# Kernel tuning notes

Measured on AMD Instinct MI355X. Metric: run time of the kernel, lower is better.

Reference implementation:

```python
import jax, jax.numpy as jnp
import numpy as np

N_P = 128          # n_particles
N_D = 3            # spatial dims (dim // n_particles)
DIM = N_P * N_D    # 384
F = 32             # n_features
H = 32             # n_hidden
B = 128            # batch
COORDS_RANGE = 5.0
EPS = 1e-6         # bgflow distances_from_vectors eps


def _edge_indices():
    # i-major ordering over all ordered pairs (i, j), i != j, matching
    # both _create_edges_indices and the off-diagonal layout of distance_vectors.
    ii, jj = np.meshgrid(np.arange(N_P), np.arange(N_P), indexing='ij')
    mask = ii != jj
    return ii[mask], jj[mask]  # each [E] with E = N_P*(N_P-1)

IDX_I, IDX_J = _edge_indices()


def setup_inputs() -> dict:
    key = jax.random.key(0)
    ks = jax.random.split(key, 12)

    def nrm(k, shape, s=0.05):
        return jax.random.normal(k, shape, jnp.float32) * s

    return dict(
        x=jax.random.normal(ks[0], (B, DIM), jnp.float32),
        h=jax.random.normal(ks[1], (B, N_P, F), jnp.float32),
        d_static=jax.random.uniform(ks[2], (B, N_P * (N_P - 1)), jnp.float32),
        # edge_network: Linear(2F+2, H), SiLU, Linear(H, F), SiLU
        e_w1=nrm(ks[3], (2 * F + 2, H)), e_b1=jnp.zeros((H,), jnp.float32),
        e_w2=nrm(ks[4], (H, F)), e_b2=jnp.zeros((F,), jnp.float32),
        # node_network: Linear(2F, H), SiLU, Linear(H, F)
        n_w1=nrm(ks[5], (2 * F, H)), n_b1=jnp.zeros((H,), jnp.float32),
        n_w2=nrm(ks[6], (H, F)), n_b2=jnp.zeros((F,), jnp.float32),
        # coord_network: Linear(F, H), SiLU, Linear(H, 1, bias=False) [xavier gain 1e-3], Tanh
        c_w1=nrm(ks[7], (F, H)), c_b1=jnp.zeros((H,), jnp.float32),
        c_w2=nrm(ks[8], (H, 1), 0.001),
        # att_mlp: Linear(F, 1), Sigmoid
        a_w=nrm(ks[9], (F, 1)), a_b=jnp.zeros((1,), jnp.float32),
    )


def reference(x, h, d_static, e_w1, e_b1, e_w2, e_b2,
              n_w1, n_b1, n_w2, n_b2, c_w1, c_b1, c_w2, a_w, a_b):
    xi = x.reshape(-1, N_P, N_D)                       # [B, n, 3]
    # distance_vectors: r_ij = x_i - x_j over ordered pairs, diagonal removed
    r = xi[:, IDX_I] - xi[:, IDX_J]                    # [B, E, 3]
    d = jnp.sqrt(jnp.sum(r * r, axis=-1) + EPS)        # [B, E]

    # edge_transformation on [h_i, h_j, d^2, d_static^2]
    hi = h[:, IDX_I]                                   # [B, E, F] gather
    hj = h[:, IDX_J]                                   # [B, E, F] gather
    ds = d_static.reshape(d.shape)
    e_in = jnp.concatenate([hi, hj, (d * d)[..., None], (ds * ds)[..., None]], axis=-1)
    m = jax.nn.silu(jax.nn.silu(e_in @ e_w1 + e_b1) @ e_w2 + e_b2)  # [B, E, F]
    m = m * jax.nn.sigmoid(m @ a_w + a_b)              # attention gate

    # coordinate update: r / (d + 1) * tanh(coord_mlp(m)), summed over neighbors
    trans = jnp.tanh(jax.nn.silu(m @ c_w1 + c_b1) @ c_w2)           # [B, E, 1]
    x_upd = (r / (d[..., None] + 1.0)) * trans                      # [B, E, 3]
    x_upd = x_upd.reshape(-1, N_P, N_P - 1, N_D).sum(axis=2)        # scatter-sum over j
    x_out = xi + x_upd * COORDS_RANGE                               # [B, n, 3]

    # node update: sum messages over neighbors, concat with h, small MLP
    m_i = m.reshape(-1, N_P, N_P - 1, F).sum(axis=2)                # [B, n, F]
    h_upd = jax.nn.silu(jnp.concatenate([h, m_i], axis=-1) @ n_w1 + n_b1) @ n_w2 + n_b2
    h_out = h + h_upd
    return x_out, h_out
```

## Files before the change

kernel.cpp:

```cpp
#include <hip/hip_runtime.h>
#include <hip/hip_bf16.h>

#define NP 128
#define NPE 127

typedef short v8s __attribute__((ext_vector_type(8)));
typedef float v4f __attribute__((ext_vector_type(4)));

#define L_HCJ  0
#define L_GEOM 4608
#define L_HCI  8704
#define L_TOT  8832

__device__ __forceinline__ float fast_rcp(float x){ return __builtin_amdgcn_rcpf(x); }
__device__ __forceinline__ float sigmoidf_(float x){ return fast_rcp(1.0f + __expf(-x)); }
__device__ __forceinline__ float siluf(float x){ return x * sigmoidf_(x); }
__device__ __forceinline__ float tanhf_fast(float x){
    return 1.0f - 2.0f * fast_rcp(1.0f + __expf(2.0f * x));
}
__device__ __forceinline__ short f2bf(float x){
    __hip_bfloat16 h = __float2bfloat16(x);
    return *reinterpret_cast<short*>(&h);
}

__global__ __launch_bounds__(256)
void eq_gnn_fused(const float* __restrict__ X, const float* __restrict__ Hin,
                  const float* __restrict__ DS,
                  const float* __restrict__ EW1, const float* __restrict__ EB1,
                  const float* __restrict__ EW2, const float* __restrict__ EB2,
                  const float* __restrict__ NW1, const float* __restrict__ NB1,
                  const float* __restrict__ NW2, const float* __restrict__ NB2,
                  const float* __restrict__ CW1, const float* __restrict__ CB1,
                  const float* __restrict__ CW2,
                  const float* __restrict__ AW,  const float* __restrict__ AB,
                  float* __restrict__ OUT)
{
    __shared__ float sm[L_TOT];
    const int tid  = threadIdx.x;
    const int lane = tid & 63;
    const int wid  = tid >> 6;
    const int m16  = lane & 15;
    const int q    = lane >> 4;
    const int bI   = blockIdx.x >> 5;
    const int grp  = blockIdx.x & 31;
    const int i    = grp * 4 + wid;
    const int node = bI * 128 + i;

    {
        v8s Aj0, Aj1;
        #pragma unroll
        for (int jj = 0; jj < 8; ++jj){
            Aj0[jj] = f2bf(EW1[(32 + q*8 + jj) * 32 + m16]);
            Aj1[jj] = f2bf(EW1[(32 + q*8 + jj) * 32 + 16 + m16]);
        }
        #pragma unroll
        for (int rr = 0; rr < 2; ++rr){
            const int row = (wid * 2 + rr) * 16 + m16;
            const float* hp = &Hin[(bI * 128 + row) * 32 + q * 8];
            const float4 h0 = *(const float4*)&hp[0];
            const float4 h1 = *(const float4*)&hp[4];
            v8s Bh;
            Bh[0]=f2bf(h0.x); Bh[1]=f2bf(h0.y); Bh[2]=f2bf(h0.z); Bh[3]=f2bf(h0.w);
            Bh[4]=f2bf(h1.x); Bh[5]=f2bf(h1.y); Bh[6]=f2bf(h1.z); Bh[7]=f2bf(h1.w);
            v4f d0 = {0.f,0.f,0.f,0.f}, d1 = {0.f,0.f,0.f,0.f};
            d0 = __builtin_amdgcn_mfma_f32_16x16x32_bf16(Aj0, Bh, d0, 0, 0, 0);
            d1 = __builtin_amdgcn_mfma_f32_16x16x32_bf16(Aj1, Bh, d1, 0, 0, 0);
            #pragma unroll
            for (int r = 0; r < 4; ++r){
                sm[L_HCJ + row * 36 + q*4 + r]      = d0[r];
                sm[L_HCJ + row * 36 + 16 + q*4 + r] = d1[r];
            }
        }
    }
    if (tid < 128){
        const int nl = tid >> 5, o = tid & 31;
        const float* hp = &Hin[(bI * 128 + grp * 4 + nl) * 32];
        float acc = EB1[o];
        #pragma unroll
        for (int k = 0; k < 32; ++k) acc = fmaf(hp[k], EW1[k * 32 + o], acc);
        sm[L_HCI + nl * 32 + o] = acc;
    }
    float* sg = &sm[L_GEOM + wid * 1024];
    const float xi0 = X[bI*384 + i*3 + 0];
    const float xi1 = X[bI*384 + i*3 + 1];
    const float xi2 = X[bI*384 + i*3 + 2];
    #pragma unroll
    for (int p = 0; p < 2; ++p){
        const int slot = lane + 64 * p;
        const int js = (slot < NPE) ? slot : 126;
        const int j = js + ((js >= i) ? 1 : 0);
        const float* xj = &X[bI*384 + j*3];
        const float r0 = xi0 - xj[0], r1 = xi1 - xj[1], r2 = xi2 - xj[2];
        const float d2 = fmaf(r0, r0, fmaf(r1, r1, fmaf(r2, r2, 1e-6f)));
        const float d  = sqrtf(d2);
        const float rinv = fast_rcp(d + 1.0f);
        const float dsv = DS[bI*16256 + i*127 + js];
        *(float4*)&sg[slot*8]     = make_float4(r0, r1, r2, rinv);
        *(float2*)&sg[slot*8 + 4] = make_float2(d2, dsv * dsv);
    }
    __syncthreads();

    v8s Aw20, Aw21, Ac0, Ac1;
    #pragma unroll
    for (int jj = 0; jj < 8; ++jj){
        Aw20[jj] = f2bf(EW2[(q*8 + jj) * 32 + m16]);
        Aw21[jj] = f2bf(EW2[(q*8 + jj) * 32 + 16 + m16]);
        const int tau = (jj < 4) ? (q*4 + jj) : (16 + q*4 + (jj - 4));
        Ac0[jj] = f2bf(CW1[tau * 32 + m16]);
        Ac1[jj] = f2bf(CW1[tau * 32 + 16 + m16]);
    }
    const float4 w64a = *(const float4*)&EW1[64*32 + q*8];
    const float4 w64b = *(const float4*)&EW1[64*32 + q*8 + 4];
    const float4 w65a = *(const float4*)&EW1[65*32 + q*8];
    const float4 w65b = *(const float4*)&EW1[65*32 + q*8 + 4];
    const float4 b2A = *(const float4*)&EB2[q*4];
    const float4 b2B = *(const float4*)&EB2[16 + q*4];
    const float4 cbA = *(const float4*)&CB1[q*4];
    const float4 cbB = *(const float4*)&CB1[16 + q*4];
    const float4 cwA = *(const float4*)&CW2[q*4];
    const float4 cwB = *(const float4*)&CW2[16 + q*4];
    const float4 awA = *(const float4*)&AW[q*4];
    const float4 awB = *(const float4*)&AW[16 + q*4];
    const float ab0 = AB[0];
    const float4 hci0 = *(const float4*)&sm[L_HCI + wid*32 + q*8];
    const float4 hci1 = *(const float4*)&sm[L_HCI + wid*32 + q*8 + 4];

    float ms[8];
    #pragma unroll
    for (int jj = 0; jj < 8; ++jj) ms[jj] = 0.f;
    float xc0 = 0.f, xc1 = 0.f, xc2 = 0.f;

    #pragma unroll 1
    for (int tl = 0; tl < 8; ++tl){
        const int e = tl * 16 + m16;
        const float valid = (e < NPE) ? 1.f : 0.f;
        const int js = (e < NPE) ? e : 126;
        const int j = js + ((js >= i) ? 1 : 0);

        const float2 dd = *(const float2*)&sg[e*8 + 4];
        const float4 hj0 = *(const float4*)&sm[L_HCJ + j*36 + q*8];
        const float4 hj1 = *(const float4*)&sm[L_HCJ + j*36 + q*8 + 4];

        v8s Bt;
        Bt[0] = f2bf(siluf(fmaf(dd.x, w64a.x, fmaf(dd.y, w65a.x, hci0.x + hj0.x))));
        Bt[1] = f2bf(siluf(fmaf(dd.x, w64a.y, fmaf(dd.y, w65a.y, hci0.y + hj0.y))));
        Bt[2] = f2bf(siluf(fmaf(dd.x, w64a.z, fmaf(dd.y, w65a.z, hci0.z + hj0.z))));
        Bt[3] = f2bf(siluf(fmaf(dd.x, w64a.w, fmaf(dd.y, w65a.w, hci0.w + hj0.w))));
        Bt[4] = f2bf(siluf(fmaf(dd.x, w64b.x, fmaf(dd.y, w65b.x, hci1.x + hj1.x))));
        Bt[5] = f2bf(siluf(fmaf(dd.x, w64b.y, fmaf(dd.y, w65b.y, hci1.y + hj1.y))));
        Bt[6] = f2bf(siluf(fmaf(dd.x, w64b.z, fmaf(dd.y, w65b.z, hci1.z + hj1.z))));
        Bt[7] = f2bf(siluf(fmaf(dd.x, w64b.w, fmaf(dd.y, w65b.w, hci1.w + hj1.w))));

        v4f c0 = {b2A.x, b2A.y, b2A.z, b2A.w};
        v4f c1 = {b2B.x, b2B.y, b2B.z, b2B.w};
        c0 = __builtin_amdgcn_mfma_f32_16x16x32_bf16(Aw20, Bt, c0, 0, 0, 0);
        c1 = __builtin_amdgcn_mfma_f32_16x16x32_bf16(Aw21, Bt, c1, 0, 0, 0);
        const float s0 = siluf(c0[0]), s1 = siluf(c0[1]), s2 = siluf(c0[2]), s3 = siluf(c0[3]);
        const float s4 = siluf(c1[0]), s5 = siluf(c1[1]), s6 = siluf(c1[2]), s7 = siluf(c1[3]);

        float lg = s0*awA.x + s1*awA.y + s2*awA.z + s3*awA.w
                 + s4*awB.x + s5*awB.y + s6*awB.z + s7*awB.w;
        lg += __shfl_xor(lg, 16, 64);
        lg += __shfl_xor(lg, 32, 64);
        const float att = sigmoidf_(lg + ab0) * valid;

        v8s Bm;
        float g;
        g = s0*att; ms[0] += g; Bm[0] = f2bf(g);
        g = s1*att; ms[1] += g; Bm[1] = f2bf(g);
        g = s2*att; ms[2] += g; Bm[2] = f2bf(g);
        g = s3*att; ms[3] += g; Bm[3] = f2bf(g);
        g = s4*att; ms[4] += g; Bm[4] = f2bf(g);
        g = s5*att; ms[5] += g; Bm[5] = f2bf(g);
        g = s6*att; ms[6] += g; Bm[6] = f2bf(g);
        g = s7*att; ms[7] += g; Bm[7] = f2bf(g);

        v4f e0 = {cbA.x, cbA.y, cbA.z, cbA.w};
        v4f e1 = {cbB.x, cbB.y, cbB.z, cbB.w};
        e0 = __builtin_amdgcn_mfma_f32_16x16x32_bf16(Ac0, Bm, e0, 0, 0, 0);
        e1 = __builtin_amdgcn_mfma_f32_16x16x32_bf16(Ac1, Bm, e1, 0, 0, 0);
        float tr = siluf(e0[0])*cwA.x + siluf(e0[1])*cwA.y + siluf(e0[2])*cwA.z + siluf(e0[3])*cwA.w
                 + siluf(e1[0])*cwB.x + siluf(e1[1])*cwB.y + siluf(e1[2])*cwB.z + siluf(e1[3])*cwB.w;
        tr += __shfl_xor(tr, 16, 64);
        tr += __shfl_xor(tr, 32, 64);

        const float4 rv = *(const float4*)&sg[e*8];
        const float coef = tanhf_fast(tr) * rv.w * valid;
        xc0 = fmaf(rv.x, coef, xc0);
        xc1 = fmaf(rv.y, coef, xc1);
        xc2 = fmaf(rv.z, coef, xc2);
    }

    #pragma unroll
    for (int jj = 0; jj < 8; ++jj){
        float v = ms[jj];
        v += __shfl_xor(v, 1, 64); v += __shfl_xor(v, 2, 64);
        v += __shfl_xor(v, 4, 64); v += __shfl_xor(v, 8, 64);
        ms[jj] = v;
    }
    {
        float v0 = xc0, v1 = xc1, v2 = xc2;
        #pragma unroll
        for (int s = 1; s < 64; s <<= 1){
            v0 += __shfl_xor(v0, s, 64);
            v1 += __shfl_xor(v1, s, 64);
            v2 += __shfl_xor(v2, s, 64);
        }
        xc0 = v0 * 0.25f; xc1 = v1 * 0.25f; xc2 = v2 * 0.25f;
    }

    if (lane < 3){
        const float xiv = (lane == 0) ? xi0 : ((lane == 1) ? xi1 : xi2);
        const float xcv = (lane == 0) ? xc0 : ((lane == 1) ? xc1 : xc2);
        OUT[bI*384 + i*3 + lane] = fmaf(xcv, 5.0f, xiv);
    }

    if (m16 == 0){
        #pragma unroll
        for (int jj = 0; jj < 8; ++jj){
            const int tau = (jj < 4) ? (q*4 + jj) : (16 + q*4 + (jj - 4));
            sg[tau] = ms[jj];
        }
    }

    const int o = lane & 31;
    const float* hp = &Hin[node * 32];
    float a1 = NB1[o];
    #pragma unroll
    for (int k = 0; k < 32; ++k) a1 = fmaf(hp[k], NW1[k * 32 + o], a1);
    #pragma unroll
    for (int k = 0; k < 32; ++k) a1 = fmaf(sg[k], NW1[(32 + k) * 32 + o], a1);
    const float s1v = siluf(a1);
    float a2 = NB2[o];
    #pragma unroll
    for (int k = 0; k < 32; ++k) a2 = fmaf(__shfl(s1v, k, 64), NW2[k * 32 + o], a2);
    if (lane < 32)
        OUT[49152 + node * 32 + o] = hp[o] + a2;
}

extern "C" void kernel_launch(void* const* d_in, const int* in_sizes, int n_in,
                              void* d_out, int out_size, void* d_ws, size_t ws_size,
                              hipStream_t stream) {
    (void)in_sizes; (void)n_in; (void)out_size; (void)d_ws; (void)ws_size;
    eq_gnn_fused<<<dim3(4096), dim3(256), 0, stream>>>(
        (const float*)d_in[0],  (const float*)d_in[1],  (const float*)d_in[2],
        (const float*)d_in[3],  (const float*)d_in[4],  (const float*)d_in[5],  (const float*)d_in[6],
        (const float*)d_in[7],  (const float*)d_in[8],  (const float*)d_in[9],  (const float*)d_in[10],
        (const float*)d_in[11], (const float*)d_in[12], (const float*)d_in[13],
        (const float*)d_in[14], (const float*)d_in[15],
        (float*)d_out);
}
```

Before: 171.0 us.

## Use 8-wave blocks, packed float2 math, exp2-based activations, split geometry LDS

Blocks now hold 8 waves (8 nodes) instead of 4, so each block computes the per-batch h_j projection table once for twice as many nodes. This halves the redundant MFMA and global-load work for that table. The SiLU, attention and coord-MLP arithmetic is regrouped into float2 vectors so the compiler can emit packed FP32 instructions. Sigmoid and tanh now use a raw exp2 builtin, and geometry storage in LDS is split into separate r/rinv and d² arrays. The larger blocks use more shared memory and registers per block, which may reduce occupancy.

New measurement: 158.7 us. -7.2%, faster.

```diff
diff --git a/kernel.cpp b/kernel.cpp
--- a/kernel.cpp
+++ b/kernel.cpp
@@ -1,29 +1,48 @@
 #include <hip/hip_runtime.h>
 #include <hip/hip_bf16.h>
 
-#define NP 128
 #define NPE 127
 
 typedef short v8s __attribute__((ext_vector_type(8)));
 typedef float v4f __attribute__((ext_vector_type(4)));
-
-#define L_HCJ  0
-#define L_GEOM 4608
-#define L_HCI  8704
-#define L_TOT  8832
+typedef float v2f __attribute__((ext_vector_type(2)));
+
+#define L_HCJ 0
+#define L_HCI 4608
+#define L_GR  4864
+#define L_GD  8960
+#define L_TOT 11008
 
 __device__ __forceinline__ float fast_rcp(float x){ return __builtin_amdgcn_rcpf(x); }
-__device__ __forceinline__ float sigmoidf_(float x){ return fast_rcp(1.0f + __expf(-x)); }
-__device__ __forceinline__ float siluf(float x){ return x * sigmoidf_(x); }
+__device__ __forceinline__ float exp2_fast(float x){
+#if __has_builtin(__builtin_amdgcn_exp2f)
+    return __builtin_amdgcn_exp2f(x);
+#else
+    return exp2f(x);
+#endif
+}
+#define LOG2E 1.44269504f
+__device__ __forceinline__ float sigmoidf_(float x){
+    return fast_rcp(1.0f + exp2_fast(-LOG2E * x));
+}
 __device__ __forceinline__ float tanhf_fast(float x){
-    return 1.0f - 2.0f * fast_rcp(1.0f + __expf(2.0f * x));
+    return fmaf(-2.0f, fast_rcp(1.0f + exp2_fast(2.0f * LOG2E * x)), 1.0f);
+}
+__device__ __forceinline__ v2f splat2(float v){ v2f r; r.x = v; r.y = v; return r; }
+__device__ __forceinline__ v2f silu2(v2f x){
+    v2f t = x * splat2(-LOG2E);
+    v2f e; e.x = exp2_fast(t.x); e.y = exp2_fast(t.y);
+    v2f d = e + splat2(1.0f);
+    v2f r; r.x = fast_rcp(d.x); r.y = fast_rcp(d.y);
+    return x * r;
 }
 __device__ __forceinline__ short f2bf(float x){
     __hip_bfloat16 h = __float2bfloat16(x);
     return *reinterpret_cast<short*>(&h);
 }
-
-__global__ __launch_bounds__(256)
+union f4u { float4 f4; v2f v2[2]; float f[4]; };
+
+__global__ __launch_bounds__(512)
 void eq_gnn_fused(const float* __restrict__ X, const float* __restrict__ Hin,
                   const float* __restrict__ DS,
                   const float* __restrict__ EW1, const float* __restrict__ EB1,
@@ -41,9 +60,9 @@
     const int wid  = tid >> 6;
     const int m16  = lane & 15;
     const int q    = lane >> 4;
-    const int bI   = blockIdx.x >> 5;
-    const int grp  = blockIdx.x & 31;
-    const int i    = grp * 4 + wid;
+    const int bI   = blockIdx.x >> 4;
+    const int grp  = blockIdx.x & 15;
+    const int i    = grp * 8 + wid;
     const int node = bI * 128 + i;
 
     {
@@ -53,34 +72,32 @@
             Aj0[jj] = f2bf(EW1[(32 + q*8 + jj) * 32 + m16]);
             Aj1[jj] = f2bf(EW1[(32 + q*8 + jj) * 32 + 16 + m16]);
         }
-        #pragma unroll
-        for (int rr = 0; rr < 2; ++rr){
-            const int row = (wid * 2 + rr) * 16 + m16;
-            const float* hp = &Hin[(bI * 128 + row) * 32 + q * 8];
-            const float4 h0 = *(const float4*)&hp[0];
-            const float4 h1 = *(const float4*)&hp[4];
-            v8s Bh;
-            Bh[0]=f2bf(h0.x); Bh[1]=f2bf(h0.y); Bh[2]=f2bf(h0.z); Bh[3]=f2bf(h0.w);
-            Bh[4]=f2bf(h1.x); Bh[5]=f2bf(h1.y); Bh[6]=f2bf(h1.z); Bh[7]=f2bf(h1.w);
-            v4f d0 = {0.f,0.f,0.f,0.f}, d1 = {0.f,0.f,0.f,0.f};
-            d0 = __builtin_amdgcn_mfma_f32_16x16x32_bf16(Aj0, Bh, d0, 0, 0, 0);
-            d1 = __builtin_amdgcn_mfma_f32_16x16x32_bf16(Aj1, Bh, d1, 0, 0, 0);
-            #pragma unroll
-            for (int r = 0; r < 4; ++r){
-                sm[L_HCJ + row * 36 + q*4 + r]      = d0[r];
-                sm[L_HCJ + row * 36 + 16 + q*4 + r] = d1[r];
-            }
-        }
-    }
-    if (tid < 128){
+        const int row = wid * 16 + m16;
+        const float* hp = &Hin[(bI * 128 + row) * 32 + q * 8];
+        const float4 h0 = *(const float4*)&hp[0];
+        const float4 h1 = *(const float4*)&hp[4];
+        v8s Bh;
+        Bh[0]=f2bf(h0.x); Bh[1]=f2bf(h0.y); Bh[2]=f2bf(h0.z); Bh[3]=f2bf(h0.w);
+        Bh[4]=f2bf(h1.x); Bh[5]=f2bf(h1.y); Bh[6]=f2bf(h1.z); Bh[7]=f2bf(h1.w);
+        v4f d0 = {0.f,0.f,0.f,0.f}, d1 = {0.f,0.f,0.f,0.f};
+        d0 = __builtin_amdgcn_mfma_f32_16x16x32_bf16(Aj0, Bh, d0, 0, 0, 0);
+        d1 = __builtin_amdgcn_mfma_f32_16x16x32_bf16(Aj1, Bh, d1, 0, 0, 0);
+        #pragma unroll
+        for (int r = 0; r < 4; ++r){
+            sm[L_HCJ + row * 36 + q*4 + r]      = d0[r];
+            sm[L_HCJ + row * 36 + 16 + q*4 + r] = d1[r];
+        }
+    }
+    if (tid < 256){
         const int nl = tid >> 5, o = tid & 31;
-        const float* hp = &Hin[(bI * 128 + grp * 4 + nl) * 32];
+        const float* hp = &Hin[(bI * 128 + grp * 8 + nl) * 32];
         float acc = EB1[o];
         #pragma unroll
         for (int k = 0; k < 32; ++k) acc = fmaf(hp[k], EW1[k * 32 + o], acc);
         sm[L_HCI + nl * 32 + o] = acc;
     }
-    float* sg = &sm[L_GEOM + wid * 1024];
+    float* sgr = &sm[L_GR + wid * 512];
+    float* sgd = &sm[L_GD + wid * 256];
     const float xi0 = X[bI*384 + i*3 + 0];
     const float xi1 = X[bI*384 + i*3 + 1];
     const float xi2 = X[bI*384 + i*3 + 2];
@@ -95,8 +112,8 @@
         const float d  = sqrtf(d2);
         const float rinv = fast_rcp(d + 1.0f);
         const float dsv = DS[bI*16256 + i*127 + js];
-        *(float4*)&sg[slot*8]     = make_float4(r0, r1, r2, rinv);
-        *(float2*)&sg[slot*8 + 4] = make_float2(d2, dsv * dsv);
+        *(float4*)&sgr[slot*4] = make_float4(r0, r1, r2, rinv);
+        *(float2*)&sgd[slot*2] = make_float2(d2, dsv * dsv);
     }
     __syncthreads();
 
@@ -109,25 +126,26 @@
         Ac0[jj] = f2bf(CW1[tau * 32 + m16]);
         Ac1[jj] = f2bf(CW1[tau * 32 + 16 + m16]);
     }
-    const float4 w64a = *(const float4*)&EW1[64*32 + q*8];
-    const float4 w64b = *(const float4*)&EW1[64*32 + q*8 + 4];
-    const float4 w65a = *(const float4*)&EW1[65*32 + q*8];
-    const float4 w65b = *(const float4*)&EW1[65*32 + q*8 + 4];
+    f4u w64a, w64b, w65a, w65b, hcia, hcib, awa, awb, cwa, cwb;
+    w64a.f4 = *(const float4*)&EW1[64*32 + q*8];
+    w64b.f4 = *(const float4*)&EW1[64*32 + q*8 + 4];
+    w65a.f4 = *(const float4*)&EW1[65*32 + q*8];
+    w65b.f4 = *(const float4*)&EW1[65*32 + q*8 + 4];
+    hcia.f4 = *(const float4*)&sm[L_HCI + wid*32 + q*8];
+    hcib.f4 = *(const float4*)&sm[L_HCI + wid*32 + q*8 + 4];
+    awa.f4  = *(const float4*)&AW[q*4];
+    awb.f4  = *(const float4*)&AW[16 + q*4];
+    cwa.f4  = *(const float4*)&CW2[q*4];
+    cwb.f4  = *(const float4*)&CW2[16 + q*4];
     const float4 b2A = *(const float4*)&EB2[q*4];
     const float4 b2B = *(const float4*)&EB2[16 + q*4];
     const float4 cbA = *(const float4*)&CB1[q*4];
     const float4 cbB = *(const float4*)&CB1[16 + q*4];
-    const float4 cwA = *(const float4*)&CW2[q*4];
-    const float4 cwB = *(const float4*)&CW2[16 + q*4];
-    const float4 awA = *(const float4*)&AW[q*4];
-    const float4 awB = *(const float4*)&AW[16 + q*4];
     const float ab0 = AB[0];
-    const float4 hci0 = *(const float4*)&sm[L_HCI + wid*32 + q*8];
-    const float4 hci1 = *(const float4*)&sm[L_HCI + wid*32 + q*8 + 4];
-
-    float ms[8];
-    #pragma unroll
-    for (int jj = 0; jj < 8; ++jj) ms[jj] = 0.f;
+
+    v2f ms2[4];
+    #pragma unroll
+    for (int g = 0; g < 4; ++g) ms2[g] = splat2(0.f);
     float xc0 = 0.f, xc1 = 0.f, xc2 = 0.f;
 
     #pragma unroll 1
@@ -137,66 +155,95 @@
         const int js = (e < NPE) ? e : 126;
         const int j = js + ((js >= i) ? 1 : 0);
 
-        const float2 dd = *(const float2*)&sg[e*8 + 4];
-        const float4 hj0 = *(const float4*)&sm[L_HCJ + j*36 + q*8];
-        const float4 hj1 = *(const float4*)&sm[L_HCJ + j*36 + q*8 + 4];
-
+        const float2 dd = *(const float2*)&sgd[e*2];
+        f4u hjA, hjB;
+        hjA.f4 = *(const float4*)&sm[L_HCJ + j*36 + q*8];
+        hjB.f4 = *(const float4*)&sm[L_HCJ + j*36 + q*8 + 4];
+        const v2f d2s  = splat2(dd.x);
+        const v2f ds2s = splat2(dd.y);
+
+        v2f t01, t23, t45, t67;
+        {
+            v2f z;
+            z = hcia.v2[0] + hjA.v2[0];
+            z = __builtin_elementwise_fma(d2s, w64a.v2[0], z);
+            z = __builtin_elementwise_fma(ds2s, w65a.v2[0], z);
+            t01 = silu2(z);
+            z = hcia.v2[1] + hjA.v2[1];
+            z = __builtin_elementwise_fma(d2s, w64a.v2[1], z);
+            z = __builtin_elementwise_fma(ds2s, w65a.v2[1], z);
+            t23 = silu2(z);
+            z = hcib.v2[0] + hjB.v2[0];
+            z = __builtin_elementwise_fma(d2s, w64b.v2[0], z);
+            z = __builtin_elementwise_fma(ds2s, w65b.v2[0], z);
+            t45 = silu2(z);
+            z = hcib.v2[1] + hjB.v2[1];
+            z = __builtin_elementwise_fma(d2s, w64b.v2[1], z);
+            z = __builtin_elementwise_fma(ds2s, w65b.v2[1], z);
+            t67 = silu2(z);
+        }
         v8s Bt;
-        Bt[0] = f2bf(siluf(fmaf(dd.x, w64a.x, fmaf(dd.y, w65a.x, hci0.x + hj0.x))));
-        Bt[1] = f2bf(siluf(fmaf(dd.x, w64a.y, fmaf(dd.y, w65a.y, hci0.y + hj0.y))));
-        Bt[2] = f2bf(siluf(fmaf(dd.x, w64a.z, fmaf(dd.y, w65a.z, hci0.z + hj0.z))));
-        Bt[3] = f2bf(siluf(fmaf(dd.x, w64a.w, fmaf(dd.y, w65a.w, hci0.w + hj0.w))));
-        Bt[4] = f2bf(siluf(fmaf(dd.x, w64b.x, fmaf(dd.y, w65b.x, hci1.x + hj1.x))));
-        Bt[5] = f2bf(siluf(fmaf(dd.x, w64b.y, fmaf(dd.y, w65b.y, hci1.y + hj1.y))));
-        Bt[6] = f2bf(siluf(fmaf(dd.x, w64b.z, fmaf(dd.y, w65b.z, hci1.z + hj1.z))));
-        Bt[7] = f2bf(siluf(fmaf(dd.x, w64b.w, fmaf(dd.y, w65b.w, hci1.w + hj1.w))));
+        Bt[0]=f2bf(t01.x); Bt[1]=f2bf(t01.y); Bt[2]=f2bf(t23.x); Bt[3]=f2bf(t23.y);
+        Bt[4]=f2bf(t45.x); Bt[5]=f2bf(t45.y); Bt[6]=f2bf(t67.x); Bt[7]=f2bf(t67.y);
 
         v4f c0 = {b2A.x, b2A.y, b2A.z, b2A.w};
         v4f c1 = {b2B.x, b2B.y, b2B.z, b2B.w};
         c0 = __builtin_amdgcn_mfma_f32_16x16x32_bf16(Aw20, Bt, c0, 0, 0, 0);
         c1 = __builtin_amdgcn_mfma_f32_16x16x32_bf16(Aw21, Bt, c1, 0, 0, 0);
-        const float s0 = siluf(c0[0]), s1 = siluf(c0[1]), s2 = siluf(c0[2]), s3 = siluf(c0[3]);
-        const float s4 = siluf(c1[0]), s5 = siluf(c1[1]), s6 = siluf(c1[2]), s7 = siluf(c1[3]);
-
-        float lg = s0*awA.x + s1*awA.y + s2*awA.z + s3*awA.w
-                 + s4*awB.x + s5*awB.y + s6*awB.z + s7*awB.w;
+        v2f sa, sb, sc, sd;
+        { v2f z; z.x=c0[0]; z.y=c0[1]; sa = silu2(z); }
+        { v2f z; z.x=c0[2]; z.y=c0[3]; sb = silu2(z); }
+        { v2f z; z.x=c1[0]; z.y=c1[1]; sc = silu2(z); }
+        { v2f z; z.x=c1[2]; z.y=c1[3]; sd = silu2(z); }
+
+        v2f lgv = sa * awa.v2[0];
+        lgv = __builtin_elementwise_fma(sb, awa.v2[1], lgv);
+        lgv = __builtin_elementwise_fma(sc, awb.v2[0], lgv);
+        lgv = __builtin_elementwise_fma(sd, awb.v2[1], lgv);
+        float lg = lgv.x + lgv.y;
         lg += __shfl_xor(lg, 16, 64);
         lg += __shfl_xor(lg, 32, 64);
         const float att = sigmoidf_(lg + ab0) * valid;
-
+        const v2f atts = splat2(att);
+
+        const v2f g0 = sa * atts, g1 = sb * atts, g2 = sc * atts, g3 = sd * atts;
+        ms2[0] += g0; ms2[1] += g1; ms2[2] += g2; ms2[3] += g3;
         v8s Bm;
-        float g;
-        g = s0*att; ms[0] += g; Bm[0] = f2bf(g);
-        g = s1*att; ms[1] += g; Bm[1] = f2bf(g);
-        g = s2*att; ms[2] += g; Bm[2] = f2bf(g);
-        g = s3*att; ms[3] += g; Bm[3] = f2bf(g);
-        g = s4*att; ms[4] += g; Bm[4] = f2bf(g);
-        g = s5*att; ms[5] += g; Bm[5] = f2bf(g);
-        g = s6*att; ms[6] += g; Bm[6] = f2bf(g);
-        g = s7*att; ms[7] += g; Bm[7] = f2bf(g);
+        Bm[0]=f2bf(g0.x); Bm[1]=f2bf(g0.y); Bm[2]=f2bf(g1.x); Bm[3]=f2bf(g1.y);
+        Bm[4]=f2bf(g2.x); Bm[5]=f2bf(g2.y); Bm[6]=f2bf(g3.x); Bm[7]=f2bf(g3.y);
 
         v4f e0 = {cbA.x, cbA.y, cbA.z, cbA.w};
         v4f e1 = {cbB.x, cbB.y, cbB.z, cbB.w};
         e0 = __builtin_amdgcn_mfma_f32_16x16x32_bf16(Ac0, Bm, e0, 0, 0, 0);
         e1 = __builtin_amdgcn_mfma_f32_16x16x32_bf16(Ac1, Bm, e1, 0, 0, 0);
-        float tr = siluf(e0[0])*cwA.x + siluf(e0[1])*cwA.y + siluf(e0[2])*cwA.z + siluf(e0[3])*cwA.w
-                 + siluf(e1[0])*cwB.x + siluf(e1[1])*cwB.y + siluf(e1[2])*cwB.z + siluf(e1[3])*cwB.w;
+        v2f ca, cb, cc, cd;
+        { v2f z; z.x=e0[0]; z.y=e0[1]; ca = silu2(z); }
+        { v2f z; z.x=e0[2]; z.y=e0[3]; cb = silu2(z); }
+        { v2f z; z.x=e1[0]; z.y=e1[1]; cc = silu2(z); }
+        { v2f z; z.x=e1[2]; z.y=e1[3]; cd = silu2(z); }
+        v2f trv = ca * cwa.v2[0];
+        trv = __builtin_elementwise_fma(cb, cwa.v2[1], trv);
+        trv = __builtin_elementwise_fma(cc, cwb.v2[0], trv);
+        trv = __builtin_elementwise_fma(cd, cwb.v2[1], trv);
+        float tr = trv.x + trv.y;
         tr += __shfl_xor(tr, 16, 64);
         tr += __shfl_xor(tr, 32, 64);
 
-        const float4 rv = *(const float4*)&sg[e*8];
+        const float4 rv = *(const float4*)&sgr[e*4];
         const float coef = tanhf_fast(tr) * rv.w * valid;
         xc0 = fmaf(rv.x, coef, xc0);
         xc1 = fmaf(rv.y, coef, xc1);
         xc2 = fmaf(rv.z, coef, xc2);
     }
 
+    float msv[8] = {ms2[0].x, ms2[0].y, ms2[1].x, ms2[1].y,
+                    ms2[2].x, ms2[2].y, ms2[3].x, ms2[3].y};
     #pragma unroll
     for (int jj = 0; jj < 8; ++jj){
-        float v = ms[jj];
+        float v = msv[jj];
         v += __shfl_xor(v, 1, 64); v += __shfl_xor(v, 2, 64);
         v += __shfl_xor(v, 4, 64); v += __shfl_xor(v, 8, 64);
-        ms[jj] = v;
+        msv[jj] = v;
     }
     {
         float v0 = xc0, v1 = xc1, v2 = xc2;
@@ -219,7 +266,7 @@
         #pragma unroll
         for (int jj = 0; jj < 8; ++jj){
             const int tau = (jj < 4) ? (q*4 + jj) : (16 + q*4 + (jj - 4));
-            sg[tau] = ms[jj];
+            sgr[tau] = msv[jj];
         }
     }
 
@@ -229,8 +276,8 @@
     #pragma unroll
     for (int k = 0; k < 32; ++k) a1 = fmaf(hp[k], NW1[k * 32 + o], a1);
     #pragma unroll
-    for (int k = 0; k < 32; ++k) a1 = fmaf(sg[k], NW1[(32 + k) * 32 + o], a1);
-    const float s1v = siluf(a1);
+    for (int k = 0; k < 32; ++k) a1 = fmaf(sgr[k], NW1[(32 + k) * 32 + o], a1);
+    const float s1v = a1 * sigmoidf_(a1);
     float a2 = NB2[o];
     #pragma unroll
     for (int k = 0; k < 32; ++k) a2 = fmaf(__shfl(s1v, k, 64), NW2[k * 32 + o], a2);
@@ -242,7 +289,7 @@
                               void* d_out, int out_size, void* d_ws, size_t ws_size,
                               hipStream_t stream) {
     (void)in_sizes; (void)n_in; (void)out_size; (void)d_ws; (void)ws_size;
-    eq_gnn_fused<<<dim3(4096), dim3(256), 0, stream>>>(
+    eq_gnn_fused<<<dim3(2048), dim3(512), 0, stream>>>(
         (const float*)d_in[0],  (const float*)d_in[1],  (const float*)d_in[2],
         (const float*)d_in[3],  (const float*)d_in[4],  (const float*)d_in[5],  (const float*)d_in[6],
         (const float*)d_in[7],  (const float*)d_in[8],  (const float*)d_in[9],  (const float*)d_in[10],
```
